# Kernel optimization log

Hardware: AMD Instinct MI355X
Metric: run time of the kernel (lower is better)

Reference implementation:

```python
import jax, jax.numpy as jnp
import numpy as np

EPS = 1e-6

def _ste(x, xq):
    return x + jax.lax.stop_gradient(xq - x)

def rmsnorm(x, w):
    return x * jax.lax.rsqrt(jnp.mean(x * x, axis=-1, keepdims=True) + EPS) * w

def act_quant(x):
    # per-token absmax int8 quantization (BitNet b1.58)
    s = 127.0 / jnp.clip(jnp.max(jnp.abs(x), axis=-1, keepdims=True), 1e-5)
    return _ste(x, jnp.clip(jnp.round(x * s), -128, 127) / s)

def w_quant(w):
    # per-tensor mean-absmax ternary quantization
    s = 1.0 / jnp.clip(jnp.mean(jnp.abs(w)), 1e-5)
    return _ste(w, jnp.clip(jnp.round(w * s), -1, 1) / s)

def bitlinear(x, w):
    return act_quant(x) @ w_quant(w).T

def snake_beta(x, log_a, log_b):
    a = jnp.exp(log_a)
    b = jnp.exp(log_b)
    s = jnp.sin(a * x)
    return x + (1.0 / (b + 1e-9)) * s * s

def ffn(x, nw, w1, la, lb, w2):
    h = bitlinear(rmsnorm(x, nw), w1)
    return bitlinear(snake_beta(h, la, lb), w2)

def mha(x, nw, ipw, ipb, opw, opb, num_heads):
    B, T, D = x.shape
    hd = D // num_heads
    xn = rmsnorm(x, nw)
    qkv = xn @ ipw.T + ipb  # [B,T,3D]
    q, k, v = jnp.split(qkv, 3, axis=-1)
    def heads(t):
        return t.reshape(B, T, num_heads, hd).transpose(0, 2, 1, 3)  # [B,H,T,hd]
    q, k, v = heads(q), heads(k), heads(v)
    scores = jnp.einsum('bhqd,bhkd->bhqk', q, k) / jnp.sqrt(jnp.asarray(hd, x.dtype))
    attn = jax.nn.softmax(scores, axis=-1)
    o = jnp.einsum('bhqk,bhkd->bhqd', attn, v)
    o = o.transpose(0, 2, 1, 3).reshape(B, T, D)
    return o @ opw.T + opb

def conv_branch(x, nw, pw1, dw, dwb, bg, bb, bm, bv, la, lb, pw2, K):
    B, T, D = x.shape
    h = rmsnorm(x, nw)
    h = bitlinear(h, pw1)  # [B,T,2D] (1x1 BitConv1d)
    a, g = jnp.split(h, 2, axis=-1)
    h = a * jax.nn.sigmoid(g)  # GLU over channels
    hc = h.transpose(0, 2, 1)  # [B,D,T]
    hc = jax.lax.conv_general_dilated(
        hc, dw, window_strides=(1,), padding=[(K // 2, K // 2)],
        feature_group_count=D, dimension_numbers=('NCH', 'OIH', 'NCH'))
    hc = hc + dwb[None, :, None]
    hc = (hc - bm[None, :, None]) * jax.lax.rsqrt(bv[None, :, None] + 1e-5) * bg[None, :, None] + bb[None, :, None]
    h = hc.transpose(0, 2, 1)  # [B,T,D]
    h = snake_beta(h, la, lb)
    return bitlinear(h, pw2)

def setup_inputs() -> dict:
    key = jax.random.key(0)
    B, T, D, H, K = 4, 2048, 512, 8, 31
    ks = jax.random.split(key, 16)
    n = lambda k, s: (jax.random.normal(k, s, jnp.float32) * 0.02)
    d = {
        'x': jax.random.normal(ks[0], (B, T, D), jnp.float32),
        'ff1_norm_w': jnp.ones((D,), jnp.float32),
        'ff1_w1': n(ks[1], (4 * D, D)), 'ff1_a': jnp.zeros((4 * D,), jnp.float32),
        'ff1_b': jnp.zeros((4 * D,), jnp.float32), 'ff1_w2': n(ks[2], (D, 4 * D)),
        'attn_norm_w': jnp.ones((D,), jnp.float32),
        'in_proj_w': n(ks[3], (3 * D, D)), 'in_proj_b': jnp.zeros((3 * D,), jnp.float32),
        'out_proj_w': n(ks[4], (D, D)), 'out_proj_b': jnp.zeros((D,), jnp.float32),
        'conv_norm_w': jnp.ones((D,), jnp.float32),
        'pw1_w': n(ks[5], (2 * D, D)),
        'dw_w': n(ks[6], (D, 1, K)), 'dw_b': jnp.zeros((D,), jnp.float32),
        'bn_g': jnp.ones((D,), jnp.float32), 'bn_b': jnp.zeros((D,), jnp.float32),
        'bn_m': jnp.zeros((D,), jnp.float32), 'bn_v': jnp.ones((D,), jnp.float32),
        'snake_a': jnp.zeros((D,), jnp.float32), 'snake_b': jnp.zeros((D,), jnp.float32),
        'pw2_w': n(ks[7], (D, D)),
        'ff2_norm_w': jnp.ones((D,), jnp.float32),
        'ff2_w1': n(ks[8], (4 * D, D)), 'ff2_a': jnp.zeros((4 * D,), jnp.float32),
        'ff2_b': jnp.zeros((4 * D,), jnp.float32), 'ff2_w2': n(ks[9], (D, 4 * D)),
        'final_norm_w': jnp.ones((D,), jnp.float32),
    }
    return d

def reference(x, ff1_norm_w, ff1_w1, ff1_a, ff1_b, ff1_w2, attn_norm_w, in_proj_w, in_proj_b, out_proj_w, out_proj_b, conv_norm_w, pw1_w, dw_w, dw_b, bn_g, bn_b, bn_m, bn_v, snake_a, snake_b, pw2_w, ff2_norm_w, ff2_w1, ff2_a, ff2_b, ff2_w2, final_norm_w):
    H, K = 8, 31
    x = x + 0.5 * ffn(x, ff1_norm_w, ff1_w1, ff1_a, ff1_b, ff1_w2)
    x = x + mha(x, attn_norm_w, in_proj_w, in_proj_b, out_proj_w, out_proj_b, H)
    x = x + conv_branch(x, conv_norm_w, pw1_w, dw_w, dw_b, bn_g, bn_b, bn_m, bn_v, snake_a, snake_b, pw2_w, K)
    x = x + 0.5 * ffn(x, ff2_norm_w, ff2_w1, ff2_a, ff2_b, ff2_w2)
    return rmsnorm(x, final_norm_w)
```

## Files before the change

### kernel.cpp

```cpp
#include <hip/hip_runtime.h>
#include <math.h>


typedef int   v4i __attribute__((ext_vector_type(4)));
typedef float v4f __attribute__((ext_vector_type(4)));
typedef float v16f __attribute__((ext_vector_type(16)));
typedef short v8s __attribute__((ext_vector_type(8)));
typedef unsigned short u16;

#define GLOAD_LDS(g, l) __builtin_amdgcn_global_load_lds( \
    (const __attribute__((address_space(1))) void*)(g),   \
    (__attribute__((address_space(3))) void*)(l), 16, 0, 0)

__device__ __forceinline__ float blk_sum256(float v, float* sm) {
#pragma unroll
  for (int m = 32; m; m >>= 1) v += __shfl_xor(v, m);
  int w = threadIdx.x >> 6;
  __syncthreads();
  if ((threadIdx.x & 63) == 0) sm[w] = v;
  __syncthreads();
  return sm[0] + sm[1] + sm[2] + sm[3];
}

__device__ __forceinline__ float blk_max256(float v, float* sm) {
#pragma unroll
  for (int m = 32; m; m >>= 1) v = fmaxf(v, __shfl_xor(v, m));
  int w = threadIdx.x >> 6;
  __syncthreads();
  if ((threadIdx.x & 63) == 0) sm[w] = v;
  __syncthreads();
  return fmaxf(fmaxf(sm[0], sm[1]), fmaxf(sm[2], sm[3]));
}

__device__ __forceinline__ u16 f2bf(float f) {
  union { float f; unsigned u; } x;
  x.f = f;
  unsigned r = x.u + 0x7fffu + ((x.u >> 16) & 1u);
  return (u16)(r >> 16);
}

__device__ __forceinline__ float bf2f(u16 u) {
  union { unsigned u; float f; } x;
  x.u = ((unsigned)u) << 16;
  return x.f;
}

__device__ __forceinline__ void xcd_tiles(int& tx, int& ty) {
  int nx = gridDim.x;
  int flat = blockIdx.y * nx + blockIdx.x;
  int nwg = nx * gridDim.y;
  int cpx = nwg >> 3;
  int swz = (flat & 7) * cpx + (flat >> 3);
  ty = swz / nx;
  tx = swz - ty * nx;
}

__global__ __launch_bounds__(256) void wabs_stage1(
    const float* __restrict__ w0, const float* __restrict__ w1,
    const float* __restrict__ w2, const float* __restrict__ w3,
    const float* __restrict__ w4, const float* __restrict__ w5,
    const float* __restrict__ w6, float* __restrict__ part) {
  __shared__ float sm[4];
  const float* ws[7] = {w0, w1, w2, w3, w4, w5, w6};
  const int ns[7] = {1048576, 1048576, 524288, 262144, 1048576, 1048576, 786432};
  int widx = blockIdx.x >> 6;
  int chunk = blockIdx.x & 63;
  const float* w = ws[widx];
  int n = ns[widx];
  if (widx < 6) {
    float s = 0.f;
    for (int i = chunk * 256 + threadIdx.x; i < n; i += 64 * 256) s += fabsf(w[i]);
    s = blk_sum256(s, sm);
    if (threadIdx.x == 0) part[widx * 64 + chunk] = s;
  } else {
    float s = 0.f;
    for (int i = chunk * 256 + threadIdx.x; i < n; i += 64 * 256) s = fmaxf(s, fabsf(w[i]));
    s = blk_max256(s, sm);
    if (threadIdx.x == 0) part[widx * 64 + chunk] = s;
  }
}

__global__ __launch_bounds__(256) void wquant_all(
    const float* __restrict__ w0, const float* __restrict__ w1,
    const float* __restrict__ w2, const float* __restrict__ w3,
    const float* __restrict__ w4, const float* __restrict__ w5,
    const float* __restrict__ w6,
    const float* __restrict__ part, float* __restrict__ scales,
    signed char* __restrict__ out) {
  const float* ws[7] = {w0, w1, w2, w3, w4, w5, w6};
  const int ns[7] = {1048576, 1048576, 524288, 262144, 1048576, 1048576, 786432};
  const int offs[7] = {0, 1048576, 2097152, 2621440, 2883584, 3932160, 4980736};
  int widx = blockIdx.y;
  const float* w = ws[widx];
  int n = ns[widx];
  signed char* o = out + offs[widx];
  float s, clipv;
  if (widx < 6) {
    float ssum = 0.f;
#pragma unroll 8
    for (int i = 0; i < 64; ++i) ssum += part[widx * 64 + i];
    float wsc = fmaxf(ssum / (float)n, 1e-5f);
    if (blockIdx.x == 0 && threadIdx.x == 0) scales[widx] = wsc;
    s = 1.0f / wsc;
    clipv = 1.f;
  } else {
    float am = 0.f;
#pragma unroll 8
    for (int i = 0; i < 64; ++i) am = fmaxf(am, part[widx * 64 + i]);
    float step = fmaxf(am, 1e-5f) * (1.0f / 127.0f);
    if (blockIdx.x == 0 && threadIdx.x == 0) scales[widx] = step;
    s = 1.0f / step;
    clipv = 127.f;
  }
  for (int i = blockIdx.x * 256 + threadIdx.x; i < n; i += 128 * 256)
    o[i] = (signed char)(int)fminf(fmaxf(rintf(w[i] * s), -clipv), clipv);
}

__global__ __launch_bounds__(256) void wcvt_tabs(
    const float* __restrict__ op, u16* __restrict__ wb,
    const float* __restrict__ a1, const float* __restrict__ b1,
    const float* __restrict__ a2, const float* __restrict__ b2,
    float* __restrict__ tabs) {
  int bid = blockIdx.x;
  if (bid < 256) {
    int i = bid * 256 + threadIdx.x;
    float4 f = *(const float4*)(op + (size_t)i * 4);
    u16* dst = wb + (size_t)i * 4;
    dst[0] = f2bf(f.x); dst[1] = f2bf(f.y); dst[2] = f2bf(f.z); dst[3] = f2bf(f.w);
  } else {
    int i = (bid - 256) * 256 + threadIdx.x;
    if (i < 2048) {
      tabs[i] = __expf(a1[i]);
      tabs[2048 + i] = 1.0f / (__expf(b1[i]) + 1e-9f);
      tabs[4096 + i] = __expf(a2[i]);
      tabs[6144 + i] = 1.0f / (__expf(b2[i]) + 1e-9f);
    }
  }
}

__global__ __launch_bounds__(256) void rmsnorm_f32x(
    const float* __restrict__ x, const float* __restrict__ w,
    signed char* __restrict__ out8, u16* __restrict__ xbf,
    float* __restrict__ dq) {
  const int tid = threadIdx.x;
  const int lane = tid & 63, wv = tid >> 6;
  const int row = blockIdx.x * 4 + wv;
  const int c0 = lane * 8;
  const float* xr = x + (size_t)row * 512 + c0;
  float4 f0 = *(const float4*)xr;
  float4 f1 = *(const float4*)(xr + 4);
  float fin[8] = {f0.x, f0.y, f0.z, f0.w, f1.x, f1.y, f1.z, f1.w};
  v8s xb;
  float v[8];
  float ss = 0.f;
#pragma unroll
  for (int j = 0; j < 8; ++j) {
    u16 b = f2bf(fin[j]);
    xb[j] = (short)b;
    v[j] = bf2f(b);
    ss = fmaf(v[j], v[j], ss);
  }
  *(v8s*)(xbf + (size_t)row * 512 + c0) = xb;
#pragma unroll
  for (int m = 1; m < 64; m <<= 1) ss += __shfl_xor(ss, m);
  float sc = 1.0f / sqrtf(ss * (1.0f / 512.0f) + 1e-6f);
  float4 w0 = *(const float4*)(w + c0);
  float4 w1 = *(const float4*)(w + c0 + 4);
  float wv8[8] = {w0.x, w0.y, w0.z, w0.w, w1.x, w1.y, w1.z, w1.w};
  float y[8];
  float am = 0.f;
#pragma unroll
  for (int j = 0; j < 8; ++j) {
    y[j] = v[j] * sc * wv8[j];
    am = fmaxf(am, fabsf(y[j]));
  }
#pragma unroll
  for (int m = 1; m < 64; m <<= 1) am = fmaxf(am, __shfl_xor(am, m));
  float amc = fmaxf(am, 1e-5f);
  float s = 127.0f / amc;
  unsigned long long pkt = 0;
#pragma unroll
  for (int j = 0; j < 8; ++j) {
    int q = (int)rintf(y[j] * s);
    pkt |= ((unsigned long long)(unsigned char)(signed char)q) << (8 * j);
  }
  *(unsigned long long*)(out8 + (size_t)row * 512 + c0) = pkt;
  if (lane == 0) dq[row] = amc * (1.0f / 127.0f);
}

__global__ __launch_bounds__(256) void rmsnorm_wave(
    const u16* __restrict__ x, const float* __restrict__ w, int mode,
    float* __restrict__ outf, signed char* __restrict__ out8,
    u16* __restrict__ outb, float* __restrict__ dq) {
  const int tid = threadIdx.x;
  const int lane = tid & 63, wv = tid >> 6;
  const int row = blockIdx.x * 4 + wv;
  const int c0 = lane * 8;
  v8s xv = *(const v8s*)(x + (size_t)row * 512 + c0);
  float v[8];
  float ss = 0.f;
#pragma unroll
  for (int j = 0; j < 8; ++j) {
    v[j] = bf2f((u16)xv[j]);
    ss = fmaf(v[j], v[j], ss);
  }
#pragma unroll
  for (int m = 1; m < 64; m <<= 1) ss += __shfl_xor(ss, m);
  float sc = 1.0f / sqrtf(ss * (1.0f / 512.0f) + 1e-6f);
  float4 w0 = *(const float4*)(w + c0);
  float4 w1 = *(const float4*)(w + c0 + 4);
  float wv8[8] = {w0.x, w0.y, w0.z, w0.w, w1.x, w1.y, w1.z, w1.w};
  float y[8];
#pragma unroll
  for (int j = 0; j < 8; ++j) y[j] = v[j] * sc * wv8[j];
  if (mode == 0) {
    float* o = outf + (size_t)row * 512 + c0;
    *(float4*)o = make_float4(y[0], y[1], y[2], y[3]);
    *(float4*)(o + 4) = make_float4(y[4], y[5], y[6], y[7]);
  } else if (mode == 1) {
    float am = 0.f;
#pragma unroll
    for (int j = 0; j < 8; ++j) am = fmaxf(am, fabsf(y[j]));
#pragma unroll
    for (int m = 1; m < 64; m <<= 1) am = fmaxf(am, __shfl_xor(am, m));
    float amc = fmaxf(am, 1e-5f);
    float s = 127.0f / amc;
    unsigned long long pkt = 0;
#pragma unroll
    for (int j = 0; j < 8; ++j) {
      int q = (int)rintf(y[j] * s);
      pkt |= ((unsigned long long)(unsigned char)(signed char)q) << (8 * j);
    }
    *(unsigned long long*)(out8 + (size_t)row * 512 + c0) = pkt;
    if (lane == 0) dq[row] = amc * (1.0f / 127.0f);
  } else {
    v8s o;
#pragma unroll
    for (int j = 0; j < 8; ++j) o[j] = (short)f2bf(y[j]);
    *(v8s*)(outb + (size_t)row * 512 + c0) = o;
  }
}

__global__ __launch_bounds__(256) void rq2048_wave(
    const u16* __restrict__ h, signed char* __restrict__ out, float* __restrict__ dq) {
  const int tid = threadIdx.x;
  const int lane = tid & 63, wv = tid >> 6;
  const int row = blockIdx.x * 4 + wv;
  const u16* hr = h + (size_t)row * 2048;
  float vals[32];
  float am = 0.f;
#pragma unroll
  for (int g = 0; g < 4; ++g) {
    int c0 = g * 512 + lane * 8;
    v8s hv = *(const v8s*)(hr + c0);
#pragma unroll
    for (int j = 0; j < 8; ++j) {
      float v = bf2f((u16)hv[j]);
      vals[g * 8 + j] = v;
      am = fmaxf(am, fabsf(v));
    }
  }
#pragma unroll
  for (int m = 1; m < 64; m <<= 1) am = fmaxf(am, __shfl_xor(am, m));
  float amc = fmaxf(am, 1e-5f);
  float s = 127.0f / amc;
#pragma unroll
  for (int g = 0; g < 4; ++g) {
    unsigned long long pkt = 0;
#pragma unroll
    for (int j = 0; j < 8; ++j) {
      int q = (int)rintf(vals[g * 8 + j] * s);
      pkt |= ((unsigned long long)(unsigned char)(signed char)q) << (8 * j);
    }
    *(unsigned long long*)(out + (size_t)row * 2048 + g * 512 + lane * 8) = pkt;
  }
  if (lane == 0) dq[row] = amc * (1.0f / 127.0f);
}

__global__ __launch_bounds__(256) void rowquant_wave(
    const u16* __restrict__ in, signed char* __restrict__ out, float* __restrict__ dq) {
  const int tid = threadIdx.x;
  const int lane = tid & 63, wv = tid >> 6;
  const int row = blockIdx.x * 4 + wv;
  const int c0 = lane * 8;
  v8s xv = *(const v8s*)(in + (size_t)row * 512 + c0);
  float v[8];
  float am = 0.f;
#pragma unroll
  for (int j = 0; j < 8; ++j) {
    v[j] = bf2f((u16)xv[j]);
    am = fmaxf(am, fabsf(v[j]));
  }
#pragma unroll
  for (int m = 1; m < 64; m <<= 1) am = fmaxf(am, __shfl_xor(am, m));
  float amc = fmaxf(am, 1e-5f);
  float s = 127.0f / amc;
  unsigned long long pkt = 0;
#pragma unroll
  for (int j = 0; j < 8; ++j) {
    int q = (int)rintf(v[j] * s);
    pkt |= ((unsigned long long)(unsigned char)(signed char)q) << (8 * j);
  }
  *(unsigned long long*)(out + (size_t)row * 512 + c0) = pkt;
  if (lane == 0) dq[row] = amc * (1.0f / 127.0f);
}

template <int BN, int OM>
__global__ __launch_bounds__(256) void gemm_i8_t(
    const signed char* __restrict__ A, const signed char* __restrict__ B,
    const float* __restrict__ wsp, const float* __restrict__ adq,
    const u16* __restrict__ resid, float rscale,
    u16* __restrict__ outb, int N, int K,
    const float* __restrict__ ta, const float* __restrict__ tb,
    const float* __restrict__ bias) {
  constexpr int JF = BN / 32;
  __shared__ signed char As[16384];
  __shared__ signed char Bs[BN * 128];
  const int tid = threadIdx.x;
  int txc, tyc;
  xcd_tiles(txc, tyc);
  const int m0 = tyc << 7;
  const int n0 = txc * BN;
  const int lane = tid & 63;
  const int wv = tid >> 6;
  const int wr = (wv >> 1) << 6, wc = (wv & 1) * (16 * JF);
  const int r15 = lane & 15, khi = lane >> 4;
  const int srow = tid >> 3;
  const int sslot = (tid & 7) ^ (srow & 7);
  const signed char* Ag = A + (size_t)(m0 + srow) * K + sslot * 16;
  const signed char* Bg = B + (size_t)(n0 + srow) * K + sslot * 16;
  const size_t row32 = (size_t)32 * K;

  int aoff[4][2], boff[JF][2];
#pragma unroll
  for (int i = 0; i < 4; ++i) {
    int r = wr + i * 16 + r15;
#pragma unroll
    for (int s = 0; s < 2; ++s)
      aoff[i][s] = r * 128 + (((s << 2) + khi) ^ (r & 7)) * 16;
  }
#pragma unroll
  for (int j = 0; j < JF; ++j) {
    int c = wc + j * 16 + r15;
#pragma unroll
    for (int s = 0; s < 2; ++s)
      boff[j][s] = c * 128 + (((s << 2) + khi) ^ (c & 7)) * 16;
  }
  v4i acc[4][JF] = {};
  for (int k0 = 0; k0 < K; k0 += 128) {
    __syncthreads();
#pragma unroll
    for (int c = 0; c < 4; ++c)
      GLOAD_LDS(Ag + c * row32 + k0, As + c * 4096 + tid * 16);
#pragma unroll
    for (int c = 0; c < BN / 32; ++c)
      GLOAD_LDS(Bg + c * row32 + k0, Bs + c * 4096 + tid * 16);
    __syncthreads();
    v4i a[4][2], b[JF][2];
#pragma unroll
    for (int i = 0; i < 4; ++i) {
      a[i][0] = *(const v4i*)(As + aoff[i][0]);
      a[i][1] = *(const v4i*)(As + aoff[i][1]);
    }
#pragma unroll
    for (int j = 0; j < JF; ++j) {
      b[j][0] = *(const v4i*)(Bs + boff[j][0]);
      b[j][1] = *(const v4i*)(Bs + boff[j][1]);
    }
#pragma unroll
    for (int i = 0; i < 4; ++i)
#pragma unroll
      for (int j = 0; j < JF; ++j) {
        acc[i][j] = __builtin_amdgcn_mfma_i32_16x16x64_i8(a[i][0], b[j][0], acc[i][j], 0, 0, 0);
        acc[i][j] = __builtin_amdgcn_mfma_i32_16x16x64_i8(a[i][1], b[j][1], acc[i][j], 0, 0, 0);
      }
  }
  const float wsc = *wsp;
#pragma unroll
  for (int i = 0; i < 4; ++i) {
    int rb = m0 + wr + i * 16 + (khi << 2);
    float dqv[4];
#pragma unroll
    for (int rr = 0; rr < 4; ++rr) dqv[rr] = adq[rb + rr] * wsc;
#pragma unroll
    for (int j = 0; j < JF; ++j) {
      int col = n0 + wc + j * 16 + r15;
      float sa, sib, bv;
      if constexpr (OM == 2) { sa = ta[col]; sib = tb[col]; }
      if constexpr (OM == 3) { bv = bias[col]; }
#pragma unroll
      for (int rr = 0; rr < 4; ++rr) {
        float v = (float)acc[i][j][rr] * dqv[rr];
        if constexpr (OM == 3) {
          v += bv;
          int rowb = rb + rr;
          int tin = rowb & 31;
          int seg = col >> 9;
          int cc = col & 511;
          int h2 = cc >> 6, d = cc & 63;
          if (seg == 0) v *= 0.18033688011112042f;
          size_t base = ((size_t)(((rowb >> 11) * 8 + h2) * 64 + ((rowb & 2047) >> 5))) * 6144;
          size_t off;
          if (seg == 0)
            off = (size_t)(8 + (d >> 4)) * 512 + ((((d >> 3) & 1) << 5) + tin) * 8 + (d & 7);
          else if (seg == 1)
            off = (size_t)(d >> 4) * 512 + ((((d >> 3) & 1) << 5) + tin) * 8 + (d & 7);
          else
            off = (size_t)(4 + ((d >> 5) << 1) + (tin >> 4)) * 512 +
                  ((((tin >> 3) & 1) << 5) + (d & 31)) * 8 + (tin & 7);
          outb[base + off] = f2bf(v);
        } else {
          size_t idx = (size_t)(rb + rr) * N + col;
          if constexpr (OM == 0) {
            outb[idx] = f2bf(v);
          } else if constexpr (OM == 1) {
            outb[idx] = f2bf(fmaf(rscale, v, bf2f(resid[idx])));
          } else {
            float sn = __sinf(sa * v);
            outb[idx] = f2bf(v + sn * sn * sib);
          }
        }
      }
    }
  }
}

template <int BN, int OM>
__global__ __launch_bounds__(256) void gemm_bf16_t(
    const u16* __restrict__ A, const u16* __restrict__ B,
    const float* __restrict__ bias, const u16* __restrict__ resid,
    u16* __restrict__ outb, int N, int K) {
  constexpr int JF = BN / 32;
  __shared__ signed char As[8192];
  __shared__ signed char Bs[BN * 64];
  const int tid = threadIdx.x;
  int txc, tyc;
  xcd_tiles(txc, tyc);
  const int m0 = tyc << 7;
  const int n0 = txc * BN;
  const int lane = tid & 63;
  const int wv = tid >> 6;
  const int wr = (wv >> 1) << 6, wc = (wv & 1) * (16 * JF);
  const int r15 = lane & 15, khi = lane >> 4;
  const int srow = tid >> 2;
  const int sslot = (tid & 3) ^ ((srow >> 1) & 3);
  const int K2 = K * 2;
  const signed char* Ag = (const signed char*)A + (size_t)(m0 + srow) * K2 + sslot * 16;
  const signed char* Bg = (const signed char*)B + (size_t)(n0 + srow) * K2 + sslot * 16;
  const size_t half = (size_t)64 * K2;

  int aoff[4], boff[JF];
#pragma unroll
  for (int i = 0; i < 4; ++i) {
    int r = wr + i * 16 + r15;
    aoff[i] = r * 64 + ((khi ^ ((r >> 1) & 3)) << 4);
  }
#pragma unroll
  for (int j = 0; j < JF; ++j) {
    int c = wc + j * 16 + r15;
    boff[j] = c * 64 + ((khi ^ ((c >> 1) & 3)) << 4);
  }
  v4f acc[4][JF] = {};
  for (int kb = 0; kb < K2; kb += 64) {
    __syncthreads();
    GLOAD_LDS(Ag + kb, As + tid * 16);
    GLOAD_LDS(Ag + half + kb, As + 4096 + tid * 16);
    GLOAD_LDS(Bg + kb, Bs + tid * 16);
    if constexpr (BN == 128) GLOAD_LDS(Bg + half + kb, Bs + 4096 + tid * 16);
    __syncthreads();
    v8s a[4], b[JF];
#pragma unroll
    for (int i = 0; i < 4; ++i) a[i] = *(const v8s*)(As + aoff[i]);
#pragma unroll
    for (int j = 0; j < JF; ++j) b[j] = *(const v8s*)(Bs + boff[j]);
#pragma unroll
    for (int i = 0; i < 4; ++i)
#pragma unroll
      for (int j = 0; j < JF; ++j)
        acc[i][j] = __builtin_amdgcn_mfma_f32_16x16x32_bf16(a[i], b[j], acc[i][j], 0, 0, 0);
  }
#pragma unroll
  for (int i = 0; i < 4; ++i) {
    int rb = m0 + wr + i * 16 + (khi << 2);
#pragma unroll
    for (int j = 0; j < JF; ++j) {
      int col = n0 + wc + j * 16 + r15;
      float bv = bias[col];
#pragma unroll
      for (int rr = 0; rr < 4; ++rr) {
        size_t idx = (size_t)(rb + rr) * N + col;
        float v = acc[i][j][rr] + bv;
        if constexpr (OM == 0) outb[idx] = f2bf(v);
        else outb[idx] = f2bf(bf2f(resid[idx]) + v);
      }
    }
  }
}

__global__ __launch_bounds__(256) void attn32(
    const u16* __restrict__ kvqp, u16* __restrict__ attno) {
  __shared__ u16 KV[2][4096];
  const int tid = threadIdx.x;
  const int lane = tid & 63;
  const int wv = tid >> 6;
  const int l31 = lane & 31;
  const int hi = lane >> 5;
  const int flat = blockIdx.y * 16 + blockIdx.x;
  const int qg = flat >> 5;
  const int bh = (flat & 7) | (((flat >> 3) & 3) << 3);
  const int b = bh >> 3, h = bh & 7;
  const int qt = qg * 4 + wv;
  const int q0 = qt << 5;

  v8s qf[4];
  {
    const u16* qb = kvqp + ((size_t)(bh * 64 + qt)) * 6144 + lane * 8;
#pragma unroll
    for (int ks = 0; ks < 4; ++ks) qf[ks] = *(const v8s*)(qb + (8 + ks) * 512);
  }
  v16f o0 = {}, o1 = {};
  float l_run = 0.f;

  const u16* tb = kvqp + ((size_t)(bh * 64)) * 6144;

  GLOAD_LDS(tb + tid * 8, &KV[0][tid * 8]);
  GLOAD_LDS(tb + 2048 + tid * 8, &KV[0][2048 + tid * 8]);
  __syncthreads();

  int cur = 0;
#pragma unroll 2
  for (int t = 0; t < 64; ++t) {
    if (t < 63) {
      const u16* nb = tb + (size_t)(t + 1) * 6144;
      GLOAD_LDS(nb + tid * 8, &KV[cur ^ 1][tid * 8]);
      GLOAD_LDS(nb + 2048 + tid * 8, &KV[cur ^ 1][2048 + tid * 8]);
    }
    v8s kf[4], vf[4];
#pragma unroll
    for (int ks = 0; ks < 4; ++ks) kf[ks] = *(const v8s*)(&KV[cur][ks * 512 + lane * 8]);
#pragma unroll
    for (int j = 0; j < 4; ++j) vf[j] = *(const v8s*)(&KV[cur][2048 + j * 512 + lane * 8]);

    __builtin_amdgcn_s_setprio(1);
    v16f sacc = {};
#pragma unroll
    for (int ks = 0; ks < 4; ++ks)
      sacc = __builtin_amdgcn_mfma_f32_32x32x16_bf16(kf[ks], qf[ks], sacc, 0, 0, 0);
    __builtin_amdgcn_s_setprio(0);

    float s[16];
#pragma unroll
    for (int r = 0; r < 16; ++r) s[r] = exp2f(sacc[r]);

    {
      float a0 = (s[0] + s[1]) + (s[2] + s[3]);
      float a1 = (s[4] + s[5]) + (s[6] + s[7]);
      float a2 = (s[8] + s[9]) + (s[10] + s[11]);
      float a3 = (s[12] + s[13]) + (s[14] + s[15]);
      float ls = (a0 + a1) + (a2 + a3);
      float tsw = ls;
      asm("v_permlane32_swap_b32 %0, %1" : "+v"(tsw), "+v"(ls));
      l_run += ls + tsw;
    }

    unsigned pk[8];
#pragma unroll
    for (int g = 0; g < 8; ++g) {
      unsigned u;
      asm("v_cvt_pk_bf16_f32 %0, %1, %2" : "=v"(u) : "v"(s[2 * g]), "v"(s[2 * g + 1]));
      pk[g] = u;
    }
    asm("v_permlane32_swap_b32 %0, %1" : "+v"(pk[2]), "+v"(pk[0]));
    asm("v_permlane32_swap_b32 %0, %1" : "+v"(pk[3]), "+v"(pk[1]));
    asm("v_permlane32_swap_b32 %0, %1" : "+v"(pk[6]), "+v"(pk[4]));
    asm("v_permlane32_swap_b32 %0, %1" : "+v"(pk[7]), "+v"(pk[5]));
    v4i w0, w1;
    w0[0] = pk[0]; w0[1] = pk[1]; w0[2] = pk[2]; w0[3] = pk[3];
    w1[0] = pk[4]; w1[1] = pk[5]; w1[2] = pk[6]; w1[3] = pk[7];
    v8s pf0 = *(v8s*)&w0;
    v8s pf1 = *(v8s*)&w1;

    __builtin_amdgcn_s_setprio(1);
    o0 = __builtin_amdgcn_mfma_f32_32x32x16_bf16(vf[0], pf0, o0, 0, 0, 0);
    o0 = __builtin_amdgcn_mfma_f32_32x32x16_bf16(vf[1], pf1, o0, 0, 0, 0);
    o1 = __builtin_amdgcn_mfma_f32_32x32x16_bf16(vf[2], pf0, o1, 0, 0, 0);
    o1 = __builtin_amdgcn_mfma_f32_32x32x16_bf16(vf[3], pf1, o1, 0, 0, 0);
    __builtin_amdgcn_s_setprio(0);

    __syncthreads();
    cur ^= 1;
  }

  float inv = 1.0f / l_run;
  u16* orow = attno + (size_t)(b * 2048 + q0 + l31) * 512 + h * 64;
#pragma unroll
  for (int dt = 0; dt < 2; ++dt) {
#pragma unroll
    for (int g = 0; g < 8; ++g) {
      int d = dt * 32 + ((2 * g) & 3) + 8 * (g >> 1) + 4 * hi;
      float a = (dt ? o1[2 * g] : o0[2 * g]) * inv;
      float bv = (dt ? o1[2 * g + 1] : o0[2 * g + 1]) * inv;
      unsigned u;
      asm("v_cvt_pk_bf16_f32 %0, %1, %2" : "=v"(u) : "v"(a), "v"(bv));
      *(unsigned*)(orow + d) = u;
    }
  }
}

__global__ __launch_bounds__(256) void dwconv_fused(
    const u16* __restrict__ g3, const float* __restrict__ dww,
    const float* __restrict__ dwb, const float* __restrict__ bng,
    const float* __restrict__ bnb, const float* __restrict__ bnm,
    const float* __restrict__ bnv, const float* __restrict__ la,
    const float* __restrict__ lb, u16* __restrict__ outp) {
  __shared__ float IN[160 * 64];
  __shared__ float WT[1984];
  __shared__ float PRM[4][64];
  const int tid = threadIdx.x;
  const int cg = blockIdx.x << 6;
  const int t0 = blockIdx.y << 7;
  const int bb = blockIdx.z;

  if (tid < 64) {
    int c = cg + tid;
    float sc = bng[c] / sqrtf(bnv[c] + 1e-5f);
    PRM[0][tid] = sc;
    PRM[1][tid] = (dwb[c] - bnm[c]) * sc + bnb[c];
    PRM[2][tid] = __expf(la[c]);
    PRM[3][tid] = 1.0f / (__expf(lb[c]) + 1e-9f);
  }
  for (int i = tid; i < 1984; i += 256) WT[i] = dww[cg * 31 + i];

#pragma unroll
  for (int p = 0; p < 5; ++p) {
    int r = p * 32 + (tid >> 3);
    int t = t0 - 16 + r;
    int c8 = (tid & 7) << 3;
    float4 lo = make_float4(0.f, 0.f, 0.f, 0.f);
    float4 hv = make_float4(0.f, 0.f, 0.f, 0.f);
    if (t >= 0 && t < 2048) {
      const u16* rp = g3 + ((size_t)(bb * 2048 + t)) * 1024 + cg + c8;
      v8s a8 = *(const v8s*)rp;
      v8s g8 = *(const v8s*)(rp + 512);
      float va[8];
#pragma unroll
      for (int j = 0; j < 8; ++j) {
        float fa = bf2f((u16)a8[j]);
        float fg = bf2f((u16)g8[j]);
        va[j] = fa / (1.f + __expf(-fg));
      }
      lo = make_float4(va[0], va[1], va[2], va[3]);
      hv = make_float4(va[4], va[5], va[6], va[7]);
    }
    *(float4*)&IN[r * 64 + c8] = lo;
    *(float4*)&IN[r * 64 + c8 + 4] = hv;
  }
  __syncthreads();

  const int ch = tid & 63;
  const int tg = tid >> 6;
  const float sc = PRM[0][ch], sh = PRM[1][ch], sa = PRM[2][ch], sib = PRM[3][ch];
  float w[31];
#pragma unroll
  for (int k = 0; k < 31; ++k) w[k] = WT[ch * 31 + k];

  for (int pass = 0; pass < 4; ++pass) {
    int tl = pass * 32 + tg * 8;
    float x[38];
#pragma unroll
    for (int i = 0; i < 38; ++i) x[i] = IN[(tl + 1 + i) * 64 + ch];
    float acc[8] = {0.f, 0.f, 0.f, 0.f, 0.f, 0.f, 0.f, 0.f};
#pragma unroll
    for (int k = 0; k < 31; ++k)
#pragma unroll
      for (int j = 0; j < 8; ++j) acc[j] = fmaf(x[k + j], w[k], acc[j]);
#pragma unroll
    for (int j = 0; j < 8; ++j) {
      float v = acc[j] * sc + sh;
      float s = __sinf(sa * v);
      v += s * s * sib;
      outp[((size_t)(bb * 2048 + t0 + tl + j)) * 512 + cg + ch] = f2bf(v);
    }
  }
}

extern "C" void kernel_launch(void* const* d_in, const int* in_sizes, int n_in,
                              void* d_out, int out_size, void* d_ws, size_t ws_size,
                              hipStream_t stream) {
  const float* x_in = (const float*)d_in[0];
  const float* ff1_norm_w = (const float*)d_in[1];
  const float* ff1_w1 = (const float*)d_in[2];
  const float* ff1_a = (const float*)d_in[3];
  const float* ff1_b = (const float*)d_in[4];
  const float* ff1_w2 = (const float*)d_in[5];
  const float* attn_norm_w = (const float*)d_in[6];
  const float* in_proj_w = (const float*)d_in[7];
  const float* in_proj_b = (const float*)d_in[8];
  const float* out_proj_w = (const float*)d_in[9];
  const float* out_proj_b = (const float*)d_in[10];
  const float* conv_norm_w = (const float*)d_in[11];
  const float* pw1_w = (const float*)d_in[12];
  const float* dw_w = (const float*)d_in[13];
  const float* dw_b = (const float*)d_in[14];
  const float* bn_g = (const float*)d_in[15];
  const float* bn_b = (const float*)d_in[16];
  const float* bn_m = (const float*)d_in[17];
  const float* bn_v = (const float*)d_in[18];
  const float* snake_a = (const float*)d_in[19];
  const float* snake_b = (const float*)d_in[20];
  const float* pw2_w = (const float*)d_in[21];
  const float* ff2_norm_w = (const float*)d_in[22];
  const float* ff2_w1 = (const float*)d_in[23];
  const float* ff2_a = (const float*)d_in[24];
  const float* ff2_b = (const float*)d_in[25];
  const float* ff2_w2 = (const float*)d_in[26];
  const float* final_norm_w = (const float*)d_in[27];
  float* out = (float*)d_out;

  char* ws = (char*)d_ws;
  u16* x_bf = (u16*)(ws + 0);
  u16* x_cur = (u16*)(ws + 8388608);
  u16* kvqp = (u16*)(ws + 41943040);
  u16* attno = (u16*)(ws + 100663296);
  u16* h_b = (u16*)(ws + 16777216);
  u16* g3b = (u16*)(ws + 16777216);
  u16* convout = (u16*)(ws + 50331648);
  signed char* a8a = (signed char*)(ws + 83886080);
  signed char* a8b = (signed char*)(ws + 88080384);
  signed char* wq = (signed char*)(ws + 113246208);
  signed char* wq_w1 = wq;
  signed char* wq_w2 = wq + 1048576;
  signed char* wq_p1 = wq + 2097152;
  signed char* wq_p2 = wq + 2621440;
  signed char* wq_f21 = wq + 2883584;
  signed char* wq_f22 = wq + 3932160;
  signed char* wq_ip = wq + 4980736;
  u16* wb = (u16*)(ws + 119013376);
  u16* wb_op = wb;
  float* scales = (float*)(ws + 120324096);
  float* partials = (float*)(ws + 120324352);
  float* ascale = (float*)(ws + 120325888);
  float* tabs = (float*)(ws + 120358912);

  wabs_stage1<<<448, 256, 0, stream>>>(ff1_w1, ff1_w2, pw1_w, pw2_w, ff2_w1, ff2_w2,
                                       in_proj_w, partials);
  wquant_all<<<dim3(128, 7), 256, 0, stream>>>(ff1_w1, ff1_w2, pw1_w, pw2_w, ff2_w1, ff2_w2,
                                               in_proj_w, partials, scales, wq);
  wcvt_tabs<<<264, 256, 0, stream>>>(out_proj_w, wb, ff1_a, ff1_b, ff2_a, ff2_b, tabs);

  rmsnorm_f32x<<<2048, 256, 0, stream>>>(x_in, ff1_norm_w, a8a, x_bf, ascale);
  gemm_i8_t<128, 2><<<dim3(16, 64), 256, 0, stream>>>(
      a8a, wq_w1, scales + 0, ascale, nullptr, 1.0f, h_b, 2048, 512, tabs, tabs + 2048, nullptr);
  rq2048_wave<<<2048, 256, 0, stream>>>(h_b, a8b, ascale);
  gemm_i8_t<64, 1><<<dim3(8, 64), 256, 0, stream>>>(
      a8b, wq_w2, scales + 1, ascale, x_bf, 0.5f, x_cur, 512, 2048, nullptr, nullptr, nullptr);

  rmsnorm_wave<<<2048, 256, 0, stream>>>(x_cur, attn_norm_w, 1, nullptr, a8a, nullptr, ascale);
  gemm_i8_t<128, 3><<<dim3(12, 64), 256, 0, stream>>>(
      a8a, wq_ip, scales + 6, ascale, nullptr, 1.0f, kvqp, 1536, 512, nullptr, nullptr,
      in_proj_b);
  attn32<<<dim3(16, 32), 256, 0, stream>>>(kvqp, attno);
  gemm_bf16_t<64, 1><<<dim3(8, 64), 256, 0, stream>>>(
      attno, wb_op, out_proj_b, x_cur, x_cur, 512, 512);

  rmsnorm_wave<<<2048, 256, 0, stream>>>(x_cur, conv_norm_w, 1, nullptr, a8a, nullptr, ascale);
  gemm_i8_t<128, 0><<<dim3(8, 64), 256, 0, stream>>>(
      a8a, wq_p1, scales + 2, ascale, nullptr, 1.0f, g3b, 1024, 512, nullptr, nullptr, nullptr);
  dwconv_fused<<<dim3(8, 16, 4), 256, 0, stream>>>(g3b, dw_w, dw_b, bn_g, bn_b, bn_m, bn_v,
                                                   snake_a, snake_b, convout);
  rowquant_wave<<<2048, 256, 0, stream>>>(convout, a8a, ascale);
  gemm_i8_t<64, 1><<<dim3(8, 64), 256, 0, stream>>>(
      a8a, wq_p2, scales + 3, ascale, x_cur, 1.0f, x_cur, 512, 512, nullptr, nullptr, nullptr);

  rmsnorm_wave<<<2048, 256, 0, stream>>>(x_cur, ff2_norm_w, 1, nullptr, a8a, nullptr, ascale);
  gemm_i8_t<128, 2><<<dim3(16, 64), 256, 0, stream>>>(
      a8a, wq_f21, scales + 4, ascale, nullptr, 1.0f, h_b, 2048, 512, tabs + 4096, tabs + 6144,
      nullptr);
  rq2048_wave<<<2048, 256, 0, stream>>>(h_b, a8b, ascale);
  gemm_i8_t<64, 1><<<dim3(8, 64), 256, 0, stream>>>(
      a8b, wq_f22, scales + 5, ascale, x_cur, 0.5f, x_cur, 512, 2048, nullptr, nullptr, nullptr);

  rmsnorm_wave<<<2048, 256, 0, stream>>>(x_cur, final_norm_w, 0, out, nullptr, nullptr, nullptr);
}
```

Baseline: 290.2 us.

## Template int8 GEMM on BM, use 64x64 tiles for N=512 GEMMs; MFMA row-sum in attention

Adds a BM template parameter to the int8 GEMM so the N=512 projections can run with 64x64 tiles. This doubles their grid from 512 to 1024 blocks for better occupancy across CUs, at the cost of less tile reuse. In attention, the softmax denominator is now computed with an extra pair of MFMAs against a vector of bf16 ones instead of VALU adds and a permlane swap. That offloads the row sum to the matrix unit but sums bf16-rounded probabilities rather than fp32 ones.

```diff
diff --git a/kernel.cpp b/kernel.cpp
--- a/kernel.cpp
+++ b/kernel.cpp
@@ -305,7 +305,7 @@
   if (lane == 0) dq[row] = amc * (1.0f / 127.0f);
 }
 
-template <int BN, int OM>
+template <int BM, int BN, int OM>
 __global__ __launch_bounds__(256) void gemm_i8_t(
     const signed char* __restrict__ A, const signed char* __restrict__ B,
     const float* __restrict__ wsp, const float* __restrict__ adq,
@@ -313,17 +313,18 @@
     u16* __restrict__ outb, int N, int K,
     const float* __restrict__ ta, const float* __restrict__ tb,
     const float* __restrict__ bias) {
+  constexpr int AI = BM / 32;
   constexpr int JF = BN / 32;
-  __shared__ signed char As[16384];
+  __shared__ signed char As[BM * 128];
   __shared__ signed char Bs[BN * 128];
   const int tid = threadIdx.x;
   int txc, tyc;
   xcd_tiles(txc, tyc);
-  const int m0 = tyc << 7;
+  const int m0 = tyc * BM;
   const int n0 = txc * BN;
   const int lane = tid & 63;
   const int wv = tid >> 6;
-  const int wr = (wv >> 1) << 6, wc = (wv & 1) * (16 * JF);
+  const int wr = (wv >> 1) * (BM / 2), wc = (wv & 1) * (16 * JF);
   const int r15 = lane & 15, khi = lane >> 4;
   const int srow = tid >> 3;
   const int sslot = (tid & 7) ^ (srow & 7);
@@ -331,9 +332,9 @@
   const signed char* Bg = B + (size_t)(n0 + srow) * K + sslot * 16;
   const size_t row32 = (size_t)32 * K;
 
-  int aoff[4][2], boff[JF][2];
-#pragma unroll
-  for (int i = 0; i < 4; ++i) {
+  int aoff[AI][2], boff[JF][2];
+#pragma unroll
+  for (int i = 0; i < AI; ++i) {
     int r = wr + i * 16 + r15;
 #pragma unroll
     for (int s = 0; s < 2; ++s)
@@ -346,19 +347,19 @@
     for (int s = 0; s < 2; ++s)
       boff[j][s] = c * 128 + (((s << 2) + khi) ^ (c & 7)) * 16;
   }
-  v4i acc[4][JF] = {};
+  v4i acc[AI][JF] = {};
   for (int k0 = 0; k0 < K; k0 += 128) {
     __syncthreads();
 #pragma unroll
-    for (int c = 0; c < 4; ++c)
+    for (int c = 0; c < BM / 32; ++c)
       GLOAD_LDS(Ag + c * row32 + k0, As + c * 4096 + tid * 16);
 #pragma unroll
     for (int c = 0; c < BN / 32; ++c)
       GLOAD_LDS(Bg + c * row32 + k0, Bs + c * 4096 + tid * 16);
     __syncthreads();
-    v4i a[4][2], b[JF][2];
-#pragma unroll
-    for (int i = 0; i < 4; ++i) {
+    v4i a[AI][2], b[JF][2];
+#pragma unroll
+    for (int i = 0; i < AI; ++i) {
       a[i][0] = *(const v4i*)(As + aoff[i][0]);
       a[i][1] = *(const v4i*)(As + aoff[i][1]);
     }
@@ -368,7 +369,7 @@
       b[j][1] = *(const v4i*)(Bs + boff[j][1]);
     }
 #pragma unroll
-    for (int i = 0; i < 4; ++i)
+    for (int i = 0; i < AI; ++i)
 #pragma unroll
       for (int j = 0; j < JF; ++j) {
         acc[i][j] = __builtin_amdgcn_mfma_i32_16x16x64_i8(a[i][0], b[j][0], acc[i][j], 0, 0, 0);
@@ -377,7 +378,7 @@
   }
   const float wsc = *wsp;
 #pragma unroll
-  for (int i = 0; i < 4; ++i) {
+  for (int i = 0; i < AI; ++i) {
     int rb = m0 + wr + i * 16 + (khi << 2);
     float dqv[4];
 #pragma unroll
@@ -518,8 +519,11 @@
 #pragma unroll
     for (int ks = 0; ks < 4; ++ks) qf[ks] = *(const v8s*)(qb + (8 + ks) * 512);
   }
-  v16f o0 = {}, o1 = {};
-  float l_run = 0.f;
+  v8s ones;
+#pragma unroll
+  for (int j = 0; j < 8; ++j) ones[j] = (short)0x3F80;
+
+  v16f o0 = {}, o1 = {}, lacc = {};
 
   const u16* tb = kvqp + ((size_t)(bh * 64)) * 6144;
 
@@ -551,17 +555,6 @@
     float s[16];
 #pragma unroll
     for (int r = 0; r < 16; ++r) s[r] = exp2f(sacc[r]);
-
-    {
-      float a0 = (s[0] + s[1]) + (s[2] + s[3]);
-      float a1 = (s[4] + s[5]) + (s[6] + s[7]);
-      float a2 = (s[8] + s[9]) + (s[10] + s[11]);
-      float a3 = (s[12] + s[13]) + (s[14] + s[15]);
-      float ls = (a0 + a1) + (a2 + a3);
-      float tsw = ls;
-      asm("v_permlane32_swap_b32 %0, %1" : "+v"(tsw), "+v"(ls));
-      l_run += ls + tsw;
-    }
 
     unsigned pk[8];
 #pragma unroll
@@ -581,6 +574,8 @@
     v8s pf1 = *(v8s*)&w1;
 
     __builtin_amdgcn_s_setprio(1);
+    lacc = __builtin_amdgcn_mfma_f32_32x32x16_bf16(ones, pf0, lacc, 0, 0, 0);
+    lacc = __builtin_amdgcn_mfma_f32_32x32x16_bf16(ones, pf1, lacc, 0, 0, 0);
     o0 = __builtin_amdgcn_mfma_f32_32x32x16_bf16(vf[0], pf0, o0, 0, 0, 0);
     o0 = __builtin_amdgcn_mfma_f32_32x32x16_bf16(vf[1], pf1, o0, 0, 0, 0);
     o1 = __builtin_amdgcn_mfma_f32_32x32x16_bf16(vf[2], pf0, o1, 0, 0, 0);
@@ -591,7 +586,7 @@
     cur ^= 1;
   }
 
-  float inv = 1.0f / l_run;
+  float inv = 1.0f / lacc[0];
   u16* orow = attno + (size_t)(b * 2048 + q0 + l31) * 512 + h * 64;
 #pragma unroll
   for (int dt = 0; dt < 2; ++dt) {
@@ -749,14 +744,14 @@
   wcvt_tabs<<<264, 256, 0, stream>>>(out_proj_w, wb, ff1_a, ff1_b, ff2_a, ff2_b, tabs);
 
   rmsnorm_f32x<<<2048, 256, 0, stream>>>(x_in, ff1_norm_w, a8a, x_bf, ascale);
-  gemm_i8_t<128, 2><<<dim3(16, 64), 256, 0, stream>>>(
+  gemm_i8_t<128, 128, 2><<<dim3(16, 64), 256, 0, stream>>>(
       a8a, wq_w1, scales + 0, ascale, nullptr, 1.0f, h_b, 2048, 512, tabs, tabs + 2048, nullptr);
   rq2048_wave<<<2048, 256, 0, stream>>>(h_b, a8b, ascale);
-  gemm_i8_t<64, 1><<<dim3(8, 64), 256, 0, stream>>>(
+  gemm_i8_t<64, 64, 1><<<dim3(8, 128), 256, 0, stream>>>(
       a8b, wq_w2, scales + 1, ascale, x_bf, 0.5f, x_cur, 512, 2048, nullptr, nullptr, nullptr);
 
   rmsnorm_wave<<<2048, 256, 0, stream>>>(x_cur, attn_norm_w, 1, nullptr, a8a, nullptr, ascale);
-  gemm_i8_t<128, 3><<<dim3(12, 64), 256, 0, stream>>>(
+  gemm_i8_t<128, 128, 3><<<dim3(12, 64), 256, 0, stream>>>(
       a8a, wq_ip, scales + 6, ascale, nullptr, 1.0f, kvqp, 1536, 512, nullptr, nullptr,
       in_proj_b);
   attn32<<<dim3(16, 32), 256, 0, stream>>>(kvqp, attno);
@@ -764,20 +759,20 @@
       attno, wb_op, out_proj_b, x_cur, x_cur, 512, 512);
 
   rmsnorm_wave<<<2048, 256, 0, stream>>>(x_cur, conv_norm_w, 1, nullptr, a8a, nullptr, ascale);
-  gemm_i8_t<128, 0><<<dim3(8, 64), 256, 0, stream>>>(
+  gemm_i8_t<128, 128, 0><<<dim3(8, 64), 256, 0, stream>>>(
       a8a, wq_p1, scales + 2, ascale, nullptr, 1.0f, g3b, 1024, 512, nullptr, nullptr, nullptr);
   dwconv_fused<<<dim3(8, 16, 4), 256, 0, stream>>>(g3b, dw_w, dw_b, bn_g, bn_b, bn_m, bn_v,
                                                    snake_a, snake_b, convout);
   rowquant_wave<<<2048, 256, 0, stream>>>(convout, a8a, ascale);
-  gemm_i8_t<64, 1><<<dim3(8, 64), 256, 0, stream>>>(
+  gemm_i8_t<64, 64, 1><<<dim3(8, 128), 256, 0, stream>>>(
       a8a, wq_p2, scales + 3, ascale, x_cur, 1.0f, x_cur, 512, 512, nullptr, nullptr, nullptr);
 
   rmsnorm_wave<<<2048, 256, 0, stream>>>(x_cur, ff2_norm_w, 1, nullptr, a8a, nullptr, ascale);
-  gemm_i8_t<128, 2><<<dim3(16, 64), 256, 0, stream>>>(
+  gemm_i8_t<128, 128, 2><<<dim3(16, 64), 256, 0, stream>>>(
       a8a, wq_f21, scales + 4, ascale, nullptr, 1.0f, h_b, 2048, 512, tabs + 4096, tabs + 6144,
       nullptr);
   rq2048_wave<<<2048, 256, 0, stream>>>(h_b, a8b, ascale);
-  gemm_i8_t<64, 1><<<dim3(8, 64), 256, 0, stream>>>(
+  gemm_i8_t<64, 64, 1><<<dim3(8, 128), 256, 0, stream>>>(
       a8b, wq_f22, scales + 5, ascale, x_cur, 0.5f, x_cur, 512, 2048, nullptr, nullptr, nullptr);
 
   rmsnorm_wave<<<2048, 256, 0, stream>>>(x_cur, final_norm_w, 0, out, nullptr, nullptr, nullptr);
```

New measurement: 280.0 us. 1.04x faster.
